# Kernel optimization log

Measured on AMD Instinct MI355X. Metric: run time of the kernel, lower is better.

Reference implementation:

```python
import jax, jax.numpy as jnp
import numpy as np

B, N, D, H = 16, 4096, 768, 16
E = D // H  # head dim = 48
EPS = 1e-12  # F.normalize eps


def setup_inputs() -> dict:
    key = jax.random.key(0)
    ks = jax.random.split(key, 10)
    s = 0.02
    return {
        "x": jax.random.normal(ks[0], (B, N, D), dtype=jnp.float32),
        "wq": jax.random.normal(ks[1], (D, D), dtype=jnp.float32) * s,
        "bq": jnp.zeros((D,), dtype=jnp.float32),
        "wk": jax.random.normal(ks[2], (D, D), dtype=jnp.float32) * s,
        "bk": jnp.zeros((D,), dtype=jnp.float32),
        "wv": jax.random.normal(ks[3], (D, D), dtype=jnp.float32) * s,
        "bv": jnp.zeros((D,), dtype=jnp.float32),
        "wo": jax.random.normal(ks[4], (D, D), dtype=jnp.float32) * s,
        "bo": jnp.zeros((D,), dtype=jnp.float32),
        "tau": jnp.float32(H),  # scalar learnable temperature, init = num_heads
    }


def _l2norm_seq(t):
    # F.normalize(t, p=2, dim=1): normalize over sequence axis n of [b, n, h, e]
    nrm = jnp.sqrt(jnp.sum(t * t, axis=1, keepdims=True))
    return t / jnp.maximum(nrm, EPS)


def reference(x, wq, bq, wk, bk, wv, bv, wo, bo, tau):
    b, n, d = x.shape
    q = (x @ wq.T + bq).reshape(b, n, H, E)
    k = (x @ wk.T + bk).reshape(b, n, H, E)
    v = (x @ wv.T + bv).reshape(b, n, H, E)
    q = _l2norm_seq(q)
    k = _l2norm_seq(k)
    # cross-covariance attention over feature dim: [b, e, h, q]
    energy = jnp.einsum('bnhe,bnhq->behq', q, k)
    attn = jax.nn.softmax(energy, axis=-1)
    out = jnp.einsum('behq,bnhe->bnhq', attn / tau, v)  # [b, n, h, e]
    out = out.reshape(b, n, d)
    return out @ wo.T + bo
```

## Files before the change

### kernel.cpp

```cpp
#include <hip/hip_runtime.h>
#include <hip/hip_bf16.h>

typedef __attribute__((ext_vector_type(8))) short bf16x8_t;
typedef __attribute__((ext_vector_type(4))) float f32x4_t;
typedef __attribute__((ext_vector_type(4))) float fv4;
typedef __attribute__((ext_vector_type(4))) unsigned short us4_t;
typedef __attribute__((ext_vector_type(8))) unsigned short us8_t;

static constexpr int BB = 16, NN = 4096, DD = 768, HH = 16, EE = 48;

__device__ __forceinline__ unsigned short f2bf(float f) {
  unsigned int u = __float_as_uint(f);
  u += 0x7fffu + ((u >> 16) & 1u);
  return (unsigned short)(u >> 16);
}
__device__ __forceinline__ float bf2f(unsigned short s) {
  unsigned int u = ((unsigned int)s) << 16;
  return __uint_as_float(u);
}

__device__ __forceinline__ void load_lds16(const void* g, void* l) {
  __builtin_amdgcn_global_load_lds((const __attribute__((address_space(1))) void*)g,
                                   (__attribute__((address_space(3))) void*)l, 16, 0, 0);
}

__device__ __forceinline__ void tcast64(const float* __restrict__ src, int sld,
                                        unsigned short* __restrict__ dst, int dld, int t)
{
  __shared__ float L[64][65];
#pragma unroll
  for (int q = 0; q < 4; ++q) {
    const int fi = t + q * 256;
    const int r = fi >> 4, c4 = fi & 15;
    fv4 v = *(const fv4*)(src + (long)r * sld + c4 * 4);
    L[r][c4 * 4 + 0] = v.x; L[r][c4 * 4 + 1] = v.y;
    L[r][c4 * 4 + 2] = v.z; L[r][c4 * 4 + 3] = v.w;
  }
  __syncthreads();
#pragma unroll
  for (int q = 0; q < 2; ++q) {
    const int wi = t + q * 256;
    const int rr = wi >> 3, ng = wi & 7;
    us8_t o;
#pragma unroll
    for (int j = 0; j < 8; ++j) o[j] = f2bf(L[ng * 8 + j][rr]);
    *(us8_t*)(dst + (long)rr * dld + ng * 8) = o;
  }
  __syncthreads();
}

__global__ __launch_bounds__(256) void transpose_cast_x(
    const float* __restrict__ x, unsigned short* __restrict__ xb,
    unsigned short* __restrict__ xbT, float* __restrict__ xsum)
{
  __shared__ float L[64][65];
  __shared__ float csum[64];
  const int nx = blockIdx.x, dx = blockIdx.y, b = blockIdx.z;
  const int n0 = nx * 64, d0 = dx * 64;
  const int t = threadIdx.x;
  if (t < 64) csum[t] = 0.f;
  const float* src = x + ((long)b * NN + n0) * DD + d0;
  unsigned short* thru = xb + ((long)b * NN + n0) * DD + d0;
  unsigned short* dst = xbT + ((long)b * DD + d0) * NN + n0;
#pragma unroll
  for (int q = 0; q < 4; ++q) {
    const int fi = t + q * 256;
    const int r = fi >> 4, c4 = fi & 15;
    fv4 v = *(const fv4*)(src + (long)r * DD + c4 * 4);
    L[r][c4 * 4 + 0] = v.x; L[r][c4 * 4 + 1] = v.y;
    L[r][c4 * 4 + 2] = v.z; L[r][c4 * 4 + 3] = v.w;
    us4_t o; o.x = f2bf(v.x); o.y = f2bf(v.y); o.z = f2bf(v.z); o.w = f2bf(v.w);
    *(us4_t*)(thru + (long)r * DD + c4 * 4) = o;
  }
  __syncthreads();
#pragma unroll
  for (int q = 0; q < 2; ++q) {
    const int wi = t + q * 256;
    const int rr = wi >> 3, ng = wi & 7;
    us8_t o; float s8 = 0.f;
#pragma unroll
    for (int j = 0; j < 8; ++j) { float v = L[ng * 8 + j][rr]; o[j] = f2bf(v); s8 += v; }
    *(us8_t*)(dst + (long)rr * NN + ng * 8) = o;
    atomicAdd(&csum[rr], s8);
  }
  __syncthreads();
  if (t < 64) atomicAdd(&xsum[(long)b * DD + d0 + t], csum[t]);
}

__global__ __launch_bounds__(256) void small_cast(
    const float* __restrict__ wq, const float* __restrict__ wk, const float* __restrict__ wv,
    unsigned short* __restrict__ W2, unsigned short* __restrict__ wvT,
    float* __restrict__ zeros, float* __restrict__ xsum)
{
  const int blk = blockIdx.x, t = threadIdx.x;
  if (blk < 576) {
#pragma unroll
    for (int q = 0; q < 2; ++q) {
      long g = (long)blk * 512 + t * 2 + q;
      long e0 = g * 4;
      int row = (int)(e0 / DD), col = (int)(e0 % DD);
      const float* src = (row < DD) ? (wq + (long)row * DD + col)
                                    : (wk + (long)(row - DD) * DD + col);
      fv4 v = *(const fv4*)src;
      us4_t o; o.x = f2bf(v.x); o.y = f2bf(v.y); o.z = f2bf(v.z); o.w = f2bf(v.w);
      *(us4_t*)(W2 + e0) = o;
    }
  } else if (blk < 720) {
    const int tile = blk - 576;
    const int ti = tile / 12, tj = tile % 12;
    const int k0 = ti * 64, i0 = tj * 64;
    tcast64(wv + (long)i0 * DD + k0, DD, wvT + (long)k0 * DD + i0, DD, t);
  } else if (blk == 720) {
#pragma unroll
    for (int q = 0; q < 4; ++q) zeros[t * 4 + q] = 0.f;
  } else {
#pragma unroll
    for (int q = 0; q < 4; ++q) xsum[(long)(blk - 721) * 1024 + t * 4 + q] = 0.f;
  }
}

template<int OUT_BF16, int SYM>
__global__ __launch_bounds__(256) void gemm_bt(
    const unsigned short* __restrict__ A, int lda, long aStride,
    const unsigned short* __restrict__ Bt, int ldb, long bStride,
    void* __restrict__ Cv, int ldc, long cStride,
    const float* __restrict__ bias, long biasStride, int K,
    int perB, int nt)
{
  __shared__ unsigned short As[128 * 64];
  __shared__ unsigned short Bs[128 * 64];
  const int nwg = gridDim.x;
  const int bid = blockIdx.x;
  const int wid = (bid & 7) * (nwg >> 3) + (bid >> 3);
  const int zb = wid / perB;
  const int t0 = wid % perB;
  int i0, j0;
  if (SYM) {
    int tt = t0; i0 = 0;
    while (tt >= nt - i0) { tt -= nt - i0; ++i0; }
    j0 = i0 + tt;
  } else {
    i0 = t0 / nt; j0 = t0 % nt;
  }
  const unsigned short* Ab = A + (long)zb * aStride;
  const unsigned short* Bb = Bt + (long)zb * bStride;
  const float* bz = bias + (long)zb * biasStride;
  const long m0 = (long)i0 * 128;
  const int n0 = j0 * 128;
  const int t = threadIdx.x;
  const int wave = t >> 6, lane = t & 63;
  const int wr = wave >> 1, wc = wave & 1;

  f32x4_t acc[4][4] = {};

  const int srow = t >> 3;
  const long scol = (long)(((t & 7) ^ (srow & 7)) << 3);
  unsigned short* ldsA = As + wave * 512;
  unsigned short* ldsB = Bs + wave * 512;

  for (int kt = 0; kt < K; kt += 64) {
#pragma unroll
    for (int p = 0; p < 4; ++p) {
      load_lds16(Ab + (m0 + p * 32 + srow) * (long)lda + kt + scol, ldsA + p * 2048);
      load_lds16(Bb + (long)(n0 + p * 32 + srow) * ldb + kt + scol, ldsB + p * 2048);
    }
    __syncthreads();
#pragma unroll
    for (int kk = 0; kk < 2; ++kk) {
      const int cswz = (((kk << 2) + (lane >> 4)) ^ (lane & 7)) << 4;
      bf16x8_t af[4], bfr[4];
#pragma unroll
      for (int f = 0; f < 4; ++f) {
        af[f]  = *(const bf16x8_t*)((const char*)As + (wr * 64 + f * 16 + (lane & 15)) * 128 + cswz);
        bfr[f] = *(const bf16x8_t*)((const char*)Bs + (wc * 64 + f * 16 + (lane & 15)) * 128 + cswz);
      }
#pragma unroll
      for (int i = 0; i < 4; ++i)
#pragma unroll
        for (int j = 0; j < 4; ++j)
          acc[i][j] = __builtin_amdgcn_mfma_f32_16x16x32_bf16(af[i], bfr[j], acc[i][j], 0, 0, 0);
    }
    __syncthreads();
  }

  const int col_l = lane & 15;
  const int rbase = (lane >> 4) << 2;
#pragma unroll
  for (int i = 0; i < 4; ++i) {
    const long growb = m0 + wr * 64 + i * 16 + rbase;
#pragma unroll
    for (int j = 0; j < 4; ++j) {
      const int col = n0 + wc * 64 + j * 16 + col_l;
      if (OUT_BF16) {
        const float bcol = bz[col];
        us4_t o;
#pragma unroll
        for (int r = 0; r < 4; ++r) o[r] = f2bf(acc[i][j][r] + bcol);
        unsigned short* cb = (unsigned short*)Cv + (long)zb * cStride;
#pragma unroll
        for (int r = 0; r < 4; ++r) cb[(growb + r) * ldc + col] = o[r];
        if (SYM && i0 != j0)
          *(us4_t*)(cb + (long)col * ldc + growb) = o;
      } else {
        float* cbase = (float*)Cv + (long)zb * cStride;
#pragma unroll
        for (int r = 0; r < 4; ++r)
          cbase[(growb + r) * ldc + col] = acc[i][j][r] + bz[col];
      }
    }
  }
}

__global__ __launch_bounds__(512, 2) void gemm256(
    const unsigned short* __restrict__ A, int lda, long aStride,
    const unsigned short* __restrict__ Bt, int ldb, long bStride,
    float* __restrict__ C, int ldc, long cStride,
    const float* __restrict__ bias, long biasStride, int K,
    int perB, int nt)
{
  __shared__ unsigned short As[2 * 256 * 64];
  __shared__ unsigned short Bs[2 * 256 * 64];
  char* AsB = (char*)As;
  char* BsB = (char*)Bs;

  const int nwg = gridDim.x;
  const int bid = blockIdx.x;
  const int wid = (bid & 7) * (nwg >> 3) + (bid >> 3);
  const int zb = wid / perB;
  const int t0 = wid % perB;
  const int i0 = t0 / nt, j0 = t0 % nt;
  const unsigned short* Ab = A + (long)zb * aStride;
  const unsigned short* Bb = Bt + (long)zb * bStride;
  const float* bz = bias + (long)zb * biasStride;
  const long m0 = (long)i0 * 256;
  const int n0 = j0 * 256;
  const int t = threadIdx.x;
  const int wave = t >> 6, lane = t & 63;
  const int wr = wave >> 2, wc = wave & 3;

  f32x4_t acc[8][4] = {};

  const int srow = t >> 3;
  const long scol = (long)(((t & 7) ^ ((t >> 3) & 7)) << 3);
  const int nkt = K >> 6;

  auto STAGE = [&](int bsel, int kt) {
    const long kc = (long)kt * 64 + scol;
#pragma unroll
    for (int p = 0; p < 4; ++p) {
      load_lds16(Ab + (m0 + p * 64 + srow) * (long)lda + kc,
                 AsB + bsel * 32768 + p * 8192 + wave * 1024);
      load_lds16(Bb + (long)(n0 + p * 64 + srow) * ldb + kc,
                 BsB + bsel * 32768 + p * 8192 + wave * 1024);
    }
  };

  STAGE(0, 0);
  if (nkt > 1) STAGE(1, 1);

  const int lan15 = lane & 15, lan7 = lane & 7, kgrp = lane >> 4;

  for (int kt = 0; kt < nkt; ++kt) {
    if (kt + 1 < nkt) { asm volatile("s_waitcnt vmcnt(8)" ::: "memory"); }
    else              { asm volatile("s_waitcnt vmcnt(0)" ::: "memory"); }
    __builtin_amdgcn_sched_barrier(0);
    __builtin_amdgcn_s_barrier();
    __builtin_amdgcn_sched_barrier(0);
    const int bsel = kt & 1;
#pragma unroll
    for (int kk = 0; kk < 2; ++kk) {
      const int cswz = (((kk << 2) + kgrp) ^ lan7) << 4;
      bf16x8_t af[8], bfr[4];
#pragma unroll
      for (int mf = 0; mf < 8; ++mf)
        af[mf] = *(const bf16x8_t*)(AsB + bsel * 32768 + wr * 16384
                                    + (mf * 16 + lan15) * 128 + cswz);
#pragma unroll
      for (int nf = 0; nf < 4; ++nf) {
        const int rb = wc * 64 + nf * 16 + lan15;
        bfr[nf] = *(const bf16x8_t*)(BsB + bsel * 32768 + (rb >> 7) * 16384
                                     + (rb & 127) * 128 + cswz);
      }
#pragma unroll
      for (int mf = 0; mf < 8; ++mf)
#pragma unroll
        for (int nf = 0; nf < 4; ++nf)
          acc[mf][nf] = __builtin_amdgcn_mfma_f32_16x16x32_bf16(af[mf], bfr[nf], acc[mf][nf], 0, 0, 0);
    }
    __builtin_amdgcn_sched_barrier(0);
    __builtin_amdgcn_s_barrier();
    __builtin_amdgcn_sched_barrier(0);
    if (kt + 2 < nkt) STAGE(bsel, kt + 2);
  }

  const int rbase = (lane >> 4) << 2;
  float* Cb = C + (long)zb * cStride;
#pragma unroll
  for (int mf = 0; mf < 8; ++mf) {
    const long growb = m0 + wr * 128 + mf * 16 + rbase;
#pragma unroll
    for (int nf = 0; nf < 4; ++nf) {
      const int col = n0 + wc * 64 + nf * 16 + lan15;
      const float bcol = bz[col];
#pragma unroll
      for (int r = 0; r < 4; ++r)
        Cb[(growb + r) * ldc + col] = acc[mf][nf][r] + bcol;
    }
  }
}

#define GP_STRIDE 2464

__global__ __launch_bounds__(256) void energy_partial2(
    const unsigned short* __restrict__ T, const unsigned short* __restrict__ W2,
    float* __restrict__ Gp)
{
  __shared__ unsigned short Ts[2][48 * 128];
  __shared__ unsigned short Ws[2][48 * 128];
  __shared__ float G_sh[2448];

  const int kc = blockIdx.x, h = blockIdx.y, b = blockIdx.z;
  const int t = threadIdx.x;
  const int wave = t >> 6, lane = t & 63;

  for (int i = t; i < 2448; i += 256) G_sh[i] = 0.f;

  f32x4_t accG[3][3] = {};
  f32x4_t accQ[3] = {};
  f32x4_t accK[3] = {};

  long qoff[3];
#pragma unroll
  for (int p = 0; p < 3; ++p) {
    const int L = p * 4096 + wave * 1024 + lane * 16;
    const int e = L >> 8;
    const int blk = (L >> 4) & 15;
    const int sblk = blk ^ (e & 7);
    qoff[p] = (long)e * DD + sblk * 8;
  }
  const unsigned short* Tq = T + ((long)b * 1536 + h * 48) * DD;
  const unsigned short* Tk = Tq + (long)DD * DD;
  const unsigned short* Wq = W2 + (long)h * 48 * DD;
  const unsigned short* Wk = Wq + (long)DD * DD;

  int foff[3];
#pragma unroll
  for (int f = 0; f < 3; ++f) {
    const int e = f * 16 + (lane & 15);
    foff[f] = e * 256 + (((wave * 4 + (lane >> 4)) ^ (e & 7)) << 4);
  }
  __syncthreads();

  for (int ci = 0; ci < 3; ++ci) {
    const int col0 = kc * 384 + ci * 128;
#pragma unroll
    for (int p = 0; p < 3; ++p) {
      load_lds16(Tq + qoff[p] + col0, &Ts[0][p * 2048] + wave * 512);
      load_lds16(Tk + qoff[p] + col0, &Ts[1][p * 2048] + wave * 512);
      load_lds16(Wq + qoff[p] + col0, &Ws[0][p * 2048] + wave * 512);
      load_lds16(Wk + qoff[p] + col0, &Ws[1][p * 2048] + wave * 512);
    }
    __syncthreads();
    bf16x8_t tq[3], tk[3], wqf[3], wkf[3];
#pragma unroll
    for (int f = 0; f < 3; ++f) {
      tq[f]  = *(const bf16x8_t*)((const char*)&Ts[0][0] + foff[f]);
      tk[f]  = *(const bf16x8_t*)((const char*)&Ts[1][0] + foff[f]);
      wqf[f] = *(const bf16x8_t*)((const char*)&Ws[0][0] + foff[f]);
      wkf[f] = *(const bf16x8_t*)((const char*)&Ws[1][0] + foff[f]);
    }
#pragma unroll
    for (int i = 0; i < 3; ++i) {
      accQ[i] = __builtin_amdgcn_mfma_f32_16x16x32_bf16(tq[i], wqf[i], accQ[i], 0, 0, 0);
      accK[i] = __builtin_amdgcn_mfma_f32_16x16x32_bf16(tk[i], wkf[i], accK[i], 0, 0, 0);
#pragma unroll
      for (int j = 0; j < 3; ++j)
        accG[i][j] = __builtin_amdgcn_mfma_f32_16x16x32_bf16(tq[i], wkf[j], accG[i][j], 0, 0, 0);
    }
    __syncthreads();
  }

#pragma unroll
  for (int i = 0; i < 3; ++i)
#pragma unroll
    for (int j = 0; j < 3; ++j) {
      int e = i * 16 + ((lane >> 4) << 2);
      int qi = j * 16 + (lane & 15);
#pragma unroll
      for (int r = 0; r < 4; ++r) atomicAdd(&G_sh[(e + r) * 49 + qi], accG[i][j][r]);
    }
  if ((lane >> 4) == ((lane & 15) >> 2)) {
    int r = (lane & 15) & 3;
#pragma unroll
    for (int f = 0; f < 3; ++f) {
      atomicAdd(&G_sh[2352 + f * 16 + (lane & 15)], accQ[f][r]);
      atomicAdd(&G_sh[2400 + f * 16 + (lane & 15)], accK[f][r]);
    }
  }
  __syncthreads();

  float* out = Gp + (long)(((b * HH + h) << 1) + kc) * GP_STRIDE;
  for (int i = t; i < 2448; i += 256) out[i] = G_sh[i];
}

__global__ __launch_bounds__(256) void energy_finish2(
    const float* __restrict__ Gp, const float* __restrict__ xsum,
    const float* __restrict__ wq, const float* __restrict__ wk,
    const float* __restrict__ bq, const float* __restrict__ bk,
    const float* __restrict__ tau_p, unsigned short* __restrict__ A_out)
{
  __shared__ float G_sh[2448];
  __shared__ float vq[48], vk[48], bqs[48], bks[48];
  __shared__ int has_bias;
  const int h = blockIdx.x, b = blockIdx.y;
  const int t = threadIdx.x;

  const float* base = Gp + (long)((b * HH + h) << 1) * GP_STRIDE;
  for (int i = t; i < 2448; i += 256)
    G_sh[i] = base[i] + base[GP_STRIDE + i];
  if (t < 48) { bqs[t] = bq[h * 48 + t]; bks[t] = bk[h * 48 + t]; }
  __syncthreads();
  if (t == 0) {
    float s = 0.f;
    for (int i = 0; i < 48; ++i) s += fabsf(bqs[i]) + fabsf(bks[i]);
    has_bias = (s != 0.f);
  }
  __syncthreads();
  if (has_bias) {
    if (t < 96) {
      const int e = t < 48 ? t : t - 48;
      const float* wrow = (t < 48 ? wq : wk) + (long)(h * 48 + e) * DD;
      const float* xs = xsum + (long)b * DD;
      float s = 0.f;
      for (int g = 0; g < DD / 4; ++g) {
        fv4 a = *(const fv4*)(wrow + g * 4);
        fv4 c = *(const fv4*)(xs + g * 4);
        s += a.x * c.x + a.y * c.y + a.z * c.z + a.w * c.w;
      }
      if (t < 48) vq[e] = s; else vk[e] = s;
    }
  } else if (t < 48) { vq[t] = 0.f; vk[t] = 0.f; }
  __syncthreads();

  if (t < 48) {
    const float tau = *tau_p;
    const float nq2c = G_sh[2352 + t] + 2.f * bqs[t] * vq[t] + (float)NN * bqs[t] * bqs[t];
    const float nq = fmaxf(sqrtf(nq2c), 1e-12f);
    float row[48];
    float mx = -1e30f;
#pragma unroll 1
    for (int qi = 0; qi < 48; ++qi) {
      float nk2c = G_sh[2400 + qi] + 2.f * bks[qi] * vk[qi] + (float)NN * bks[qi] * bks[qi];
      float nk = fmaxf(sqrtf(nk2c), 1e-12f);
      float e = G_sh[t * 49 + qi] + vq[t] * bks[qi] + bqs[t] * vk[qi]
              + (float)NN * bqs[t] * bks[qi];
      float g = e / (nq * nk);
      row[qi] = g; mx = fmaxf(mx, g);
    }
    float s = 0.f;
#pragma unroll 1
    for (int qi = 0; qi < 48; ++qi) { row[qi] = __expf(row[qi] - mx); s += row[qi]; }
    const float inv = 1.f / (s * tau);
    unsigned short* dst = A_out + (((long)b * HH + h) * 48) * 64 + (long)t * 64;
#pragma unroll 1
    for (int qi = 0; qi < 48; ++qi) dst[qi] = f2bf(row[qi] * inv);
#pragma unroll 1
    for (int qi = 48; qi < 64; ++qi) dst[qi] = 0;
  }
}

__global__ __launch_bounds__(256) void build_btf(
    const unsigned short* __restrict__ A_ws, const float* __restrict__ wo,
    unsigned short* __restrict__ btf)
{
  __shared__ unsigned short Wsh[128 * 72];
  __shared__ unsigned short Ash[48 * 72];
  const int nchunk = blockIdx.x, h = blockIdx.y, b = blockIdx.z;
  const int t = threadIdx.x;
  const int wave = t >> 6, lane = t & 63;
  const int no0 = nchunk * 128;

  for (int i = t; i < 128 * 64; i += 256) {
    int r = i >> 6, c = i & 63;
    Wsh[r * 72 + c] = (c < 48) ? f2bf(wo[(long)(no0 + r) * DD + h * 48 + c]) : (unsigned short)0;
  }
  const unsigned short* Asrc = A_ws + ((long)b * HH + h) * 48 * 64;
  for (int i = t; i < 48 * 64; i += 256) {
    int r = i >> 6, c = i & 63;
    Ash[r * 72 + c] = Asrc[r * 64 + c];
  }
  __syncthreads();

  f32x4_t acc[2][3] = {};
#pragma unroll
  for (int ks = 0; ks < 2; ++ks) {
    const int k0 = ks * 32 + ((lane >> 4) << 3);
    bf16x8_t af[2], bfr[3];
#pragma unroll
    for (int mi = 0; mi < 2; ++mi)
      af[mi] = *(const bf16x8_t*)&Wsh[(wave * 32 + mi * 16 + (lane & 15)) * 72 + k0];
#pragma unroll
    for (int nj = 0; nj < 3; ++nj)
      bfr[nj] = *(const bf16x8_t*)&Ash[(nj * 16 + (lane & 15)) * 72 + k0];
#pragma unroll
    for (int mi = 0; mi < 2; ++mi)
#pragma unroll
      for (int nj = 0; nj < 3; ++nj)
        acc[mi][nj] = __builtin_amdgcn_mfma_f32_16x16x32_bf16(af[mi], bfr[nj], acc[mi][nj], 0, 0, 0);
  }

  const int col_l = lane & 15;
  const int rbase = (lane >> 4) << 2;
#pragma unroll
  for (int mi = 0; mi < 2; ++mi)
#pragma unroll
    for (int r = 0; r < 4; ++r) {
      int no = no0 + wave * 32 + mi * 16 + rbase + r;
      unsigned short* dst = btf + ((long)b * DD + no) * DD + h * 48;
#pragma unroll
      for (int nj = 0; nj < 3; ++nj)
        dst[nj * 16 + col_l] = f2bf(acc[mi][nj][r]);
    }
}

__global__ __launch_bounds__(256) void build_bias2(
    const unsigned short* __restrict__ btf, const float* __restrict__ bv,
    const float* __restrict__ bo, float* __restrict__ bias2)
{
  const int bx = blockIdx.x, b = blockIdx.y;
  const int wave = threadIdx.x >> 6, lane = threadIdx.x & 63;
  const int j = bx * 4 + wave;
  const unsigned short* row = btf + ((long)b * DD + j) * DD;
  float s = 0.f;
#pragma unroll
  for (int ii = 0; ii < 12; ++ii) {
    int i = ii * 64 + lane;
    s += bf2f(row[i]) * bv[i];
  }
#pragma unroll
  for (int off = 32; off > 0; off >>= 1) s += __shfl_down(s, off);
  if (lane == 0) bias2[(long)b * DD + j] = bo[j] + s;
}

extern "C" void kernel_launch(void* const* d_in, const int* in_sizes, int n_in,
                              void* d_out, int out_size, void* d_ws, size_t ws_size,
                              hipStream_t stream)
{
  (void)in_sizes; (void)n_in; (void)out_size;
  const float* x   = (const float*)d_in[0];
  const float* wq  = (const float*)d_in[1];
  const float* bq  = (const float*)d_in[2];
  const float* wk  = (const float*)d_in[3];
  const float* bk  = (const float*)d_in[4];
  const float* wv  = (const float*)d_in[5];
  const float* bv  = (const float*)d_in[6];
  const float* wo  = (const float*)d_in[7];
  const float* bo  = (const float*)d_in[8];
  const float* tau = (const float*)d_in[9];

  char* ws = (char*)d_ws;
  unsigned short* xb    = (unsigned short*)(ws + 0L);
  unsigned short* xbT   = (unsigned short*)(ws + 100663296L);
  unsigned short* S     = (unsigned short*)(ws + 201326592L);
  unsigned short* T     = (unsigned short*)(ws + 220200960L);
  unsigned short* W2    = (unsigned short*)(ws + 257949696L);
  unsigned short* wvT   = (unsigned short*)(ws + 260308992L);
  float*          zeros = (float*)         (ws + 261488640L);
  float*          xsum  = (float*)         (ws + 261492736L);
  float*          Gp    = (float*)         (ws + 261541888L);
  unsigned short* A_ws  = (unsigned short*)(ws + 266588160L);
  unsigned short* btf   = (unsigned short*)(ws + 268161024L);
  unsigned short* Ctf   = (unsigned short*)(ws + 287035392L);
  float*          bias2 = (float*)         (ws + 305909760L);
  if (ws_size < 305958912ULL) return;

  small_cast<<<733, 256, 0, stream>>>(wq, wk, wv, W2, wvT, zeros, xsum);
  transpose_cast_x<<<dim3(64, 12, BB), 256, 0, stream>>>(x, xb, xbT, xsum);

  gemm_bt<1, 1><<<16 * 21, 256, 0, stream>>>(
      xbT, NN, (long)DD * NN, xbT, NN, (long)DD * NN,
      S, DD, (long)DD * DD, zeros, 0L, NN, 21, 6);

  gemm_bt<1, 0><<<16 * 72, 256, 0, stream>>>(
      W2, DD, 0L, S, DD, (long)DD * DD,
      T, DD, (long)1536 * DD, zeros, 0L, DD, 72, 6);

  energy_partial2<<<dim3(2, HH, BB), 256, 0, stream>>>(T, W2, Gp);
  energy_finish2<<<dim3(HH, BB), 256, 0, stream>>>(Gp, xsum, wq, wk, bq, bk, tau, A_ws);

  build_btf<<<dim3(6, HH, BB), 256, 0, stream>>>(A_ws, wo, btf);
  build_bias2<<<dim3(192, BB), 256, 0, stream>>>(btf, bv, bo, bias2);

  gemm_bt<1, 0><<<16 * 36, 256, 0, stream>>>(
      btf, DD, (long)DD * DD, wvT, DD, 0L,
      Ctf, DD, (long)DD * DD, zeros, 0L, DD, 36, 6);

  gemm256<<<768, 512, 0, stream>>>(
      xb, DD, (long)NN * DD, Ctf, DD, (long)DD * DD,
      (float*)d_out, DD, (long)NN * DD, bias2, (long)DD, DD, 48, 3);
}
```

Measured before the change: 502.9 us.

## Retile final output GEMM to 256x128 with BK32 and higher occupancy

The final projection GEMM switches from 256x256 tiles with a K-step of 64 to 256x128 tiles with a K-step of 32. It uses a new row-paired, XOR-swizzled LDS layout and raises launch bounds to 4 blocks per CU. This cuts the accumulator registers and LDS per block, which should allow more waves per CU to hide latency, and doubles the grid to 1536 blocks for better load balance. The cost is less data reuse per tile and twice as many barriers per unit of K.

```diff
diff --git a/kernel.cpp b/kernel.cpp
--- a/kernel.cpp
+++ b/kernel.cpp
@@ -211,15 +211,15 @@
   }
 }
 
-__global__ __launch_bounds__(512, 2) void gemm256(
+__global__ __launch_bounds__(512, 4) void gemm_fin(
     const unsigned short* __restrict__ A, int lda, long aStride,
     const unsigned short* __restrict__ Bt, int ldb, long bStride,
     float* __restrict__ C, int ldc, long cStride,
     const float* __restrict__ bias, long biasStride, int K,
     int perB, int nt)
 {
-  __shared__ unsigned short As[2 * 256 * 64];
-  __shared__ unsigned short Bs[2 * 256 * 64];
+  __shared__ unsigned short As[2 * 256 * 32];
+  __shared__ unsigned short Bs[2 * 128 * 32];
   char* AsB = (char*)As;
   char* BsB = (char*)Bs;
 
@@ -233,60 +233,56 @@
   const unsigned short* Bb = Bt + (long)zb * bStride;
   const float* bz = bias + (long)zb * biasStride;
   const long m0 = (long)i0 * 256;
-  const int n0 = j0 * 256;
+  const int n0 = j0 * 128;
   const int t = threadIdx.x;
   const int wave = t >> 6, lane = t & 63;
-  const int wr = wave >> 2, wc = wave & 3;
-
-  f32x4_t acc[8][4] = {};
-
-  const int srow = t >> 3;
-  const long scol = (long)(((t & 7) ^ ((t >> 3) & 7)) << 3);
-  const int nkt = K >> 6;
+  const int wr = wave >> 1, wc = wave & 1;
+
+  f32x4_t acc[4][4] = {};
+
+  const int sh = (t >> 2) & 1;
+  const int skb = (t & 3) ^ ((t >> 3) & 3);
+  const int nkt = K >> 5;
 
   auto STAGE = [&](int bsel, int kt) {
-    const long kc = (long)kt * 64 + scol;
-#pragma unroll
-    for (int p = 0; p < 4; ++p) {
-      load_lds16(Ab + (m0 + p * 64 + srow) * (long)lda + kc,
-                 AsB + bsel * 32768 + p * 8192 + wave * 1024);
-      load_lds16(Bb + (long)(n0 + p * 64 + srow) * ldb + kc,
-                 BsB + bsel * 32768 + p * 8192 + wave * 1024);
-    }
+    const long kc = (long)kt * 32 + skb * 8;
+#pragma unroll
+    for (int p = 0; p < 2; ++p) {
+      const int rA = (((p << 6) + (t >> 3)) << 1) + sh;
+      load_lds16(Ab + (m0 + rA) * (long)lda + kc,
+                 AsB + bsel * 16384 + p * 8192 + wave * 1024);
+    }
+    const int rB = ((t >> 3) << 1) + sh;
+    load_lds16(Bb + (long)(n0 + rB) * ldb + kc,
+               BsB + bsel * 8192 + wave * 1024);
   };
 
   STAGE(0, 0);
-  if (nkt > 1) STAGE(1, 1);
-
-  const int lan15 = lane & 15, lan7 = lane & 7, kgrp = lane >> 4;
+  STAGE(1, 1);
+
+  const int lan15 = lane & 15;
+  const int l2 = lan15 >> 1;
+  const int kx = (((lane >> 4) ^ (l2 & 3)) << 4) + ((lan15 & 1) << 6);
 
   for (int kt = 0; kt < nkt; ++kt) {
-    if (kt + 1 < nkt) { asm volatile("s_waitcnt vmcnt(8)" ::: "memory"); }
+    if (kt + 1 < nkt) { asm volatile("s_waitcnt vmcnt(3)" ::: "memory"); }
     else              { asm volatile("s_waitcnt vmcnt(0)" ::: "memory"); }
     __builtin_amdgcn_sched_barrier(0);
     __builtin_amdgcn_s_barrier();
     __builtin_amdgcn_sched_barrier(0);
     const int bsel = kt & 1;
-#pragma unroll
-    for (int kk = 0; kk < 2; ++kk) {
-      const int cswz = (((kk << 2) + kgrp) ^ lan7) << 4;
-      bf16x8_t af[8], bfr[4];
-#pragma unroll
-      for (int mf = 0; mf < 8; ++mf)
-        af[mf] = *(const bf16x8_t*)(AsB + bsel * 32768 + wr * 16384
-                                    + (mf * 16 + lan15) * 128 + cswz);
-#pragma unroll
-      for (int nf = 0; nf < 4; ++nf) {
-        const int rb = wc * 64 + nf * 16 + lan15;
-        bfr[nf] = *(const bf16x8_t*)(BsB + bsel * 32768 + (rb >> 7) * 16384
-                                     + (rb & 127) * 128 + cswz);
-      }
-#pragma unroll
-      for (int mf = 0; mf < 8; ++mf)
-#pragma unroll
-        for (int nf = 0; nf < 4; ++nf)
-          acc[mf][nf] = __builtin_amdgcn_mfma_f32_16x16x32_bf16(af[mf], bfr[nf], acc[mf][nf], 0, 0, 0);
-    }
+    bf16x8_t af[4], bfr[4];
+#pragma unroll
+    for (int mf = 0; mf < 4; ++mf)
+      af[mf] = *(const bf16x8_t*)(AsB + bsel * 16384 + (wr * 32 + mf * 8 + l2) * 128 + kx);
+#pragma unroll
+    for (int nf = 0; nf < 4; ++nf)
+      bfr[nf] = *(const bf16x8_t*)(BsB + bsel * 8192 + (wc * 32 + nf * 8 + l2) * 128 + kx);
+#pragma unroll
+    for (int mf = 0; mf < 4; ++mf)
+#pragma unroll
+      for (int nf = 0; nf < 4; ++nf)
+        acc[mf][nf] = __builtin_amdgcn_mfma_f32_16x16x32_bf16(af[mf], bfr[nf], acc[mf][nf], 0, 0, 0);
     __builtin_amdgcn_sched_barrier(0);
     __builtin_amdgcn_s_barrier();
     __builtin_amdgcn_sched_barrier(0);
@@ -296,8 +292,8 @@
   const int rbase = (lane >> 4) << 2;
   float* Cb = C + (long)zb * cStride;
 #pragma unroll
-  for (int mf = 0; mf < 8; ++mf) {
-    const long growb = m0 + wr * 128 + mf * 16 + rbase;
+  for (int mf = 0; mf < 4; ++mf) {
+    const long growb = m0 + wr * 64 + mf * 16 + rbase;
 #pragma unroll
     for (int nf = 0; nf < 4; ++nf) {
       const int col = n0 + wc * 64 + nf * 16 + lan15;
@@ -595,7 +591,7 @@
       btf, DD, (long)DD * DD, wvT, DD, 0L,
       Ctf, DD, (long)DD * DD, zeros, 0L, DD, 36, 6);
 
-  gemm256<<<768, 512, 0, stream>>>(
+  gemm_fin<<<1536, 512, 0, stream>>>(
       xb, DD, (long)NN * DD, Ctf, DD, (long)DD * DD,
-      (float*)d_out, DD, (long)NN * DD, bias2, (long)DD, DD, 48, 3);
-}
+      (float*)d_out, DD, (long)NN * DD, bias2, (long)DD, DD, 96, 6);
+}
```

Result: no change. 503.9 us (+0.2%).
